# Kernel optimization log

Hardware: AMD Instinct MI355X
Metric: run time of the kernel (lower is better)

## Reference

```python
import jax, jax.numpy as jnp
import numpy as np

EMBED = 1024
HEADS = 16
HEAD_DIM = EMBED // HEADS


def setup_inputs() -> dict:
    key = jax.random.key(0)
    ks = jax.random.split(key, 12)
    B, S, D = 4, 2048, EMBED
    scale = 1.0 / np.sqrt(D)
    inp = {
        "query": jax.random.normal(ks[0], (B, S, D), dtype=jnp.float32),
        "key": jax.random.normal(ks[1], (B, S, D), dtype=jnp.float32),
        "value": jax.random.normal(ks[2], (B, S, D), dtype=jnp.float32),
        "Wq": jax.random.normal(ks[3], (D, D), dtype=jnp.float32) * scale,
        "bq": jnp.zeros((D,), dtype=jnp.float32),
        "Wk": jax.random.normal(ks[4], (D, D), dtype=jnp.float32) * scale,
        "bk": jnp.zeros((D,), dtype=jnp.float32),
        "Wv": jax.random.normal(ks[5], (D, D), dtype=jnp.float32) * scale,
        "bv": jnp.zeros((D,), dtype=jnp.float32),
        "Wo": jax.random.normal(ks[6], (D, D), dtype=jnp.float32) * scale,
        "bo": jnp.zeros((D,), dtype=jnp.float32),
    }
    return inp


def reference(query, key, value, Wq, bq, Wk, bk, Wv, bv, Wo, bo):
    B, S, D = query.shape
    H, Dh = HEADS, HEAD_DIM

    def proj(x, W, b):
        # nn.Linear: x @ W.T + b, then split heads -> [B, H, S, Dh]
        y = jnp.einsum('bsd,ed->bse', x, W) + b
        return y.reshape(B, -1, H, Dh).transpose(0, 2, 1, 3)

    q = proj(query, Wq, bq)
    k = proj(key, Wk, bk)
    v = proj(value, Wv, bv)

    attn = jnp.einsum('bhqd,bhkd->bhqk', q, k) / jnp.sqrt(jnp.float32(Dh))
    attn = jax.nn.softmax(attn, axis=-1)
    # dropout: eval mode -> identity
    out = jnp.einsum('bhqk,bhkd->bhqd', attn, v)
    out = out.transpose(0, 2, 1, 3).reshape(B, -1, D)
    out = jnp.einsum('bsd,ed->bse', out, Wo) + bo
    return out
```

## Files before the change

### kernel.cpp

```cpp
#include <hip/hip_runtime.h>
#include <hip/hip_bf16.h>

typedef unsigned short u16;
typedef unsigned int u32;
typedef float f32x4 __attribute__((ext_vector_type(4)));
typedef float f32x16 __attribute__((ext_vector_type(16)));
typedef __bf16 bf16x8 __attribute__((ext_vector_type(8)));
typedef u32 u32x2 __attribute__((ext_vector_type(2)));

#define DEV static __device__ __forceinline__

DEV u16 f2b(float f) { __bf16 h = (__bf16)f; u16 r; __builtin_memcpy(&r, &h, 2); return r; }
DEV u32 pk2(float a, float b) { return (u32)f2b(a) | ((u32)f2b(b) << 16); }
DEV bf16x8 as_bf(uint4 v) { bf16x8 r; __builtin_memcpy(&r, &v, 16); return r; }

#define GLDS(g, l) __builtin_amdgcn_global_load_lds( \
    (__attribute__((address_space(1))) void*)(g),     \
    (__attribute__((address_space(3))) void*)(l), 16, 0, 0)

DEV void wb2() { asm volatile("s_waitcnt vmcnt(2)\n\ts_barrier" ::: "memory"); }
DEV void wb4() { asm volatile("s_waitcnt vmcnt(4)\n\ts_barrier" ::: "memory"); }
DEV void wb0() { asm volatile("s_waitcnt vmcnt(0)\n\ts_barrier" ::: "memory"); }

__global__ __launch_bounds__(256) void conva3_k(const float* __restrict__ s0,
                                                const float* __restrict__ s1,
                                                const float* __restrict__ s2,
                                                u16* __restrict__ dst, int n8)
{
  const int seg = blockIdx.y;
  const float* s = seg == 0 ? s0 : (seg == 1 ? s1 : s2);
  u16* d = dst + (size_t)seg * 8388608;
  const int stride = gridDim.x * 256;
  for (int i = blockIdx.x * 256 + threadIdx.x; i < n8; i += stride) {
    const float4* p = (const float4*)(s + (size_t)i * 8);
    const float4 a = p[0], b = p[1];
    *(uint4*)(d + (size_t)i * 8) =
        make_uint4(pk2(a.x, a.y), pk2(a.z, a.w), pk2(b.x, b.y), pk2(b.z, b.w));
  }
}

__global__ __launch_bounds__(256) void convw_k(const float* __restrict__ w0,
                                               const float* __restrict__ w1,
                                               const float* __restrict__ w2,
                                               const float* __restrict__ w3,
                                               u16* __restrict__ dst)
{
  const int seg = blockIdx.x >> 9, sb = blockIdx.x & 511;
  const float* s = seg == 0 ? w0 : seg == 1 ? w1 : seg == 2 ? w2 : w3;
  const int i = sb * 256 + threadIdx.x;
  const float4* p = (const float4*)(s + (size_t)i * 8);
  const float4 a = p[0], b = p[1];
  *(uint4*)(dst + (size_t)seg * 1048576 + (size_t)i * 8) =
      make_uint4(pk2(a.x, a.y), pk2(a.z, a.w), pk2(b.x, b.y), pk2(b.z, b.w));
}

__global__ __launch_bounds__(256) void gemm_qkv(const u16* __restrict__ Ac,
                                                const u16* __restrict__ Wc,
                                                const float* __restrict__ b0,
                                                const float* __restrict__ b1,
                                                const float* __restrict__ b2,
                                                u16* __restrict__ C0,
                                                u16* __restrict__ C1,
                                                u16* __restrict__ C2,
                                                float qscale, int zq, int zv)
{
  __shared__ u16 lds[3][8192];
  const int tid = threadIdx.x;
  const int lane = tid & 63, w = tid >> 6;
  const int z = blockIdx.z;
  const int m0 = blockIdx.x * 128, e0 = blockIdx.y * 128;
  const int wrb = (w >> 1) * 4, wcb = (w & 1) * 4;

  const u16* A = Ac + (size_t)z * 8388608;
  const u16* Wp = Wc + (size_t)z * 1048576;
  const float* bias = z == 0 ? b0 : (z == 1 ? b1 : b2);
  u16* Cp = z == 0 ? C0 : (z == 1 ? C1 : C2);
  const float scale = (z == zq) ? qscale : 1.0f;
  const int cmode = (z == zv) ? 3 : 2;

  f32x4 acc[4][4];
#pragma unroll
  for (int i = 0; i < 4; i++)
#pragma unroll
    for (int j = 0; j < 4; j++)
#pragma unroll
      for (int r = 0; r < 4; r++) acc[i][j][r] = 0.f;

  const u16* gA = A  + (size_t)(m0 + w * 32 + (lane & 15)) * 1024 + (lane >> 4) * 8;
  const u16* gB = Wp + (size_t)(e0 + w * 32 + (lane & 15)) * 1024 + (lane >> 4) * 8;

#define GSTAGE(K0, BUF)                                        \
  GLDS(gA + (K0),         &lds[BUF][w * 1024]);                \
  GLDS(gA + (K0) + 16384, &lds[BUF][w * 1024 + 512]);          \
  GLDS(gB + (K0),         &lds[BUF][4096 + w * 1024]);         \
  GLDS(gB + (K0) + 16384, &lds[BUF][4096 + w * 1024 + 512]);

  GSTAGE(0, 0)
  GSTAGE(32, 1)

  const int fo = (lane >> 4) * 128 + (lane & 15) * 8;

#define GEMM_STEP(BUF)                                                         \
  {                                                                            \
    const u16* la = &lds[BUF][0];                                              \
    const u16* lb = &lds[BUF][4096];                                           \
    bf16x8 af[4], bfr[4];                                                      \
    _Pragma("unroll")                                                          \
    for (int i = 0; i < 4; i++) {                                              \
      af[i]  = as_bf(*(const uint4*)(la + (wrb + i) * 512 + fo));              \
      bfr[i] = as_bf(*(const uint4*)(lb + (wcb + i) * 512 + fo));              \
    }                                                                          \
    _Pragma("unroll")                                                          \
    for (int i = 0; i < 4; i++)                                                \
      _Pragma("unroll")                                                        \
      for (int j = 0; j < 4; j++)                                              \
        acc[i][j] = __builtin_amdgcn_mfma_f32_16x16x32_bf16(af[i], bfr[j],     \
                                                            acc[i][j], 0, 0, 0); \
  }

  for (int t = 0; t < 30; t += 3) {
    wb4(); GSTAGE((t + 2) * 32, 2) GEMM_STEP(0)
    wb4(); GSTAGE((t + 3) * 32, 0) GEMM_STEP(1)
    wb4(); GSTAGE((t + 4) * 32, 1) GEMM_STEP(2)
  }
  wb4(); GEMM_STEP(0)
  wb0(); GEMM_STEP(1)
#undef GEMM_STEP
#undef GSTAGE

  const int col = lane & 15, rb4 = (lane >> 4) * 4;
  const int wr = wrb * 16, wc = wcb * 16;
#pragma unroll
  for (int j = 0; j < 4; j++) {
    const int e = e0 + wc + j * 16 + col;
    const float bv2 = bias[e];
#pragma unroll
    for (int i = 0; i < 4; i++) {
#pragma unroll
      for (int r = 0; r < 4; r++) {
        const int m = m0 + wr + i * 16 + rb4 + r;
        const float v = (acc[i][j][r] + bv2) * scale;
        const int b = m >> 11, s = m & 2047, h = e >> 6, dh = e & 63;
        const size_t bh = (size_t)(b * 16 + h);
        if (cmode == 2) {
          const size_t idx = (((bh * 64 + (s >> 5)) * 4 + (dh >> 4)) * 64
                              + ((dh >> 3) & 1) * 32 + (s & 31)) * 8 + (dh & 7);
          Cp[idx] = f2b(v);
        } else {
          const size_t idx = ((bh * 64 + (s >> 5)) * 8 + ((s >> 4) & 1) * 4
                              + (dh >> 5) * 2 + ((s >> 3) & 1)) * 256
                             + (size_t)(dh & 31) * 8 + (s & 7);
          Cp[idx] = f2b(v);
        }
      }
    }
  }
}

__global__ __launch_bounds__(256) void gemm_o(const u16* __restrict__ A,
                                              const u16* __restrict__ W,
                                              const float* __restrict__ bias,
                                              float* __restrict__ Cp)
{
  __shared__ u16 lds[3][8192];
  const int tid = threadIdx.x;
  const int lane = tid & 63, w = tid >> 6;
  const int m0 = blockIdx.x * 128, e0 = blockIdx.y * 128;
  const int wrb = (w >> 1) * 4, wcb = (w & 1) * 4;

  f32x4 acc[4][4];
#pragma unroll
  for (int i = 0; i < 4; i++)
#pragma unroll
    for (int j = 0; j < 4; j++)
#pragma unroll
      for (int r = 0; r < 4; r++) acc[i][j][r] = 0.f;

  const u16* gA = A + (size_t)(m0 + w * 32 + (lane & 15)) * 1024 + (lane >> 4) * 8;
  const u16* gB = W + (size_t)(e0 + w * 32 + (lane & 15)) * 1024 + (lane >> 4) * 8;

#define GSTAGE(K0, BUF)                                        \
  GLDS(gA + (K0),         &lds[BUF][w * 1024]);                \
  GLDS(gA + (K0) + 16384, &lds[BUF][w * 1024 + 512]);          \
  GLDS(gB + (K0),         &lds[BUF][4096 + w * 1024]);         \
  GLDS(gB + (K0) + 16384, &lds[BUF][4096 + w * 1024 + 512]);

  GSTAGE(0, 0)
  GSTAGE(32, 1)

  const int fo = (lane >> 4) * 128 + (lane & 15) * 8;

#define GEMM_STEP(BUF)                                                         \
  {                                                                            \
    const u16* la = &lds[BUF][0];                                              \
    const u16* lb = &lds[BUF][4096];                                           \
    bf16x8 af[4], bfr[4];                                                      \
    _Pragma("unroll")                                                          \
    for (int i = 0; i < 4; i++) {                                              \
      af[i]  = as_bf(*(const uint4*)(la + (wrb + i) * 512 + fo));              \
      bfr[i] = as_bf(*(const uint4*)(lb + (wcb + i) * 512 + fo));              \
    }                                                                          \
    _Pragma("unroll")                                                          \
    for (int i = 0; i < 4; i++)                                                \
      _Pragma("unroll")                                                        \
      for (int j = 0; j < 4; j++)                                              \
        acc[i][j] = __builtin_amdgcn_mfma_f32_16x16x32_bf16(af[i], bfr[j],     \
                                                            acc[i][j], 0, 0, 0); \
  }

  for (int t = 0; t < 30; t += 3) {
    wb4(); GSTAGE((t + 2) * 32, 2) GEMM_STEP(0)
    wb4(); GSTAGE((t + 3) * 32, 0) GEMM_STEP(1)
    wb4(); GSTAGE((t + 4) * 32, 1) GEMM_STEP(2)
  }
  wb4(); GEMM_STEP(0)
  wb0(); GEMM_STEP(1)
#undef GEMM_STEP
#undef GSTAGE

  const int col = lane & 15, rb4 = (lane >> 4) * 4;
  const int wr = wrb * 16, wc = wcb * 16;
#pragma unroll
  for (int j = 0; j < 4; j++) {
    const int e = e0 + wc + j * 16 + col;
    const float bv = bias[e];
#pragma unroll
    for (int i = 0; i < 4; i++) {
#pragma unroll
      for (int r = 0; r < 4; r++) {
        const int m = m0 + wr + i * 16 + rb4 + r;
        Cp[(size_t)m * 1024 + e] = acc[i][j][r] + bv;
      }
    }
  }
}

__global__ __launch_bounds__(256, 4) void attn_k(const u16* __restrict__ Qb,
                                                 const u16* __restrict__ Kb,
                                                 const u16* __restrict__ Vb,
                                                 u16* __restrict__ O)
{
  __shared__ u16 pool[12288];
  const int tid = threadIdx.x, wv = tid >> 6, lane = tid & 63;
  const int lo = lane & 31, hi = lane >> 5;
  const int bid = blockIdx.x;
  const int xcd = bid & 7, ix = bid >> 3;
  const int bh = xcd * 8 + (ix & 7);
  const int qb = (ix >> 3) * 4 + wv;
  const int b = bh >> 4, h = bh & 15, q0 = qb * 32;

  const u16* qp = Qb + ((size_t)(bh * 64 + qb) * 4) * 512 + (size_t)lane * 8;
  bf16x8 qf[4];
#pragma unroll
  for (int c = 0; c < 4; c++) qf[c] = as_bf(*(const uint4*)(qp + c * 512));

  f32x16 a0, a1, zv;
#pragma unroll
  for (int r = 0; r < 16; r++) { a0[r] = 0.f; a1[r] = 0.f; zv[r] = 0.f; }
  float ls0 = 0.f, ls1 = 0.f;

  const u16* sgK = Kb + (size_t)bh * 131072 + wv * 512 + (size_t)lane * 8;
  const u16* sgV = Vb + (size_t)bh * 131072 + wv * 512 + (size_t)lane * 8;

#define ASTAGE(T, BUF)                                                  \
  GLDS(sgK + (size_t)(T) * 2048, pool + (BUF) * 4096 + wv * 512);       \
  GLDS(sgV + (size_t)(T) * 2048, pool + (BUF) * 4096 + 2048 + wv * 512);

  ASTAGE(0, 0)
  ASTAGE(1, 1)

#define ATTN_STEP(BUF)                                                        \
  {                                                                           \
    const u16* kl = pool + (BUF) * 4096;                                      \
    const u16* vl = kl + 2048;                                                \
    __builtin_amdgcn_s_setprio(1);                                            \
    f32x16 s = __builtin_amdgcn_mfma_f32_32x32x16_bf16(                       \
                 as_bf(*(const uint4*)(kl + lane * 8)), qf[0], zv, 0, 0, 0);  \
    _Pragma("unroll")                                                         \
    for (int c = 1; c < 4; c++)                                               \
      s = __builtin_amdgcn_mfma_f32_32x32x16_bf16(                            \
            as_bf(*(const uint4*)(kl + c * 512 + lane * 8)), qf[c], s, 0, 0, 0); \
    __builtin_amdgcn_s_setprio(0);                                            \
    _Pragma("unroll")                                                         \
    for (int r = 0; r < 16; r++) s[r] = __builtin_amdgcn_exp2f(s[r]);         \
    _Pragma("unroll")                                                         \
    for (int r = 0; r < 16; r += 2) { ls0 += s[r]; ls1 += s[r + 1]; }         \
    bf16x8 pf[2];                                                             \
    _Pragma("unroll")                                                         \
    for (int kc = 0; kc < 2; kc++) {                                          \
      const u32 A0 = pk2(s[8 * kc + 0], s[8 * kc + 1]);                       \
      const u32 A1 = pk2(s[8 * kc + 2], s[8 * kc + 3]);                       \
      const u32 B0 = pk2(s[8 * kc + 4], s[8 * kc + 5]);                       \
      const u32 B1 = pk2(s[8 * kc + 6], s[8 * kc + 7]);                       \
      u32x2 w02 = __builtin_amdgcn_permlane32_swap(A0, B0, false, false);     \
      u32x2 w13 = __builtin_amdgcn_permlane32_swap(A1, B1, false, false);     \
      pf[kc] = as_bf(make_uint4(w02[0], w13[0], w02[1], w13[1]));             \
    }                                                                         \
    __builtin_amdgcn_s_setprio(1);                                            \
    a0 = __builtin_amdgcn_mfma_f32_32x32x16_bf16(                             \
           as_bf(*(const uint4*)(vl + 0    + lane * 8)), pf[0], a0, 0, 0, 0); \
    a1 = __builtin_amdgcn_mfma_f32_32x32x16_bf16(                             \
           as_bf(*(const uint4*)(vl + 512  + lane * 8)), pf[0], a1, 0, 0, 0); \
    a0 = __builtin_amdgcn_mfma_f32_32x32x16_bf16(                             \
           as_bf(*(const uint4*)(vl + 1024 + lane * 8)), pf[1], a0, 0, 0, 0); \
    a1 = __builtin_amdgcn_mfma_f32_32x32x16_bf16(                             \
           as_bf(*(const uint4*)(vl + 1536 + lane * 8)), pf[1], a1, 0, 0, 0); \
    __builtin_amdgcn_s_setprio(0);                                            \
  }

  for (int t = 0; t < 60; t += 3) {
    wb2(); ASTAGE(t + 2, 2) ATTN_STEP(0)
    wb2(); ASTAGE(t + 3, 0) ATTN_STEP(1)
    wb2(); ASTAGE(t + 4, 1) ATTN_STEP(2)
  }
  wb2(); ASTAGE(62, 2) ATTN_STEP(0)
  wb2(); ASTAGE(63, 0) ATTN_STEP(1)
  wb2(); ATTN_STEP(2)
  wb0(); ATTN_STEP(0)
#undef ATTN_STEP
#undef ASTAGE

  __syncthreads();

  float l = ls0 + ls1;
  l += __shfl_xor(l, 32);
  const float inv = 1.f / l;
  u16* ob = pool + (wv * 32) * 72;

#pragma unroll
  for (int r = 0; r < 16; r++) {
    const int dh = (r & 3) + 8 * (r >> 2) + 4 * hi;
    ob[lo * 72 + dh]      = f2b(a0[r] * inv);
    ob[lo * 72 + dh + 32] = f2b(a1[r] * inv);
  }
  __builtin_amdgcn_s_barrier();
  const int qr = lane >> 1, hf = lane & 1;
  const u16* src = ob + qr * 72 + hf * 32;
  const uint4 r0 = *(const uint4*)(src + 0);
  const uint4 r1 = *(const uint4*)(src + 8);
  const uint4 r2 = *(const uint4*)(src + 16);
  const uint4 r3 = *(const uint4*)(src + 24);
  const size_t m = (size_t)b * 2048 + q0 + qr;
  uint4* dst = (uint4*)(O + m * 1024 + (size_t)h * 64 + hf * 32);
  dst[0] = r0; dst[1] = r1; dst[2] = r2; dst[3] = r3;
}

extern "C" void kernel_launch(void* const* d_in, const int* in_sizes, int n_in,
                              void* d_out, int out_size, void* d_ws, size_t ws_size,
                              hipStream_t stream)
{
  const float* query = (const float*)d_in[0];
  const float* key   = (const float*)d_in[1];
  const float* value = (const float*)d_in[2];
  const float* Wq = (const float*)d_in[3];
  const float* bq = (const float*)d_in[4];
  const float* Wk = (const float*)d_in[5];
  const float* bk = (const float*)d_in[6];
  const float* Wv = (const float*)d_in[7];
  const float* bv = (const float*)d_in[8];
  const float* Wo = (const float*)d_in[9];
  const float* bo = (const float*)d_in[10];

  const size_t MAT = (size_t)8192 * 1024;
  const size_t WMAT = (size_t)1024 * 1024;
  const float qscale = 0.125f * 1.4426950408889634f;
  dim3 bl(256, 1, 1);

  if (ws_size >= (6 * MAT + 4 * WMAT) * sizeof(u16)) {
    u16* Ac3 = (u16*)d_ws;
    u16* Wc  = Ac3 + 3 * MAT;
    u16* Qw  = Wc + 4 * WMAT;
    u16* Kw  = Qw + MAT;
    u16* Vw  = Kw + MAT;
    u16* Ow  = Ac3;

    hipLaunchKernelGGL(convw_k, dim3(2048), bl, 0, stream, Wq, Wk, Wv, Wo, Wc);
    hipLaunchKernelGGL(conva3_k, dim3(2048, 3), bl, 0, stream,
                       query, key, value, Ac3, (int)(MAT / 8));
    hipLaunchKernelGGL(gemm_qkv, dim3(64, 8, 3), bl, 0, stream,
                       Ac3, Wc, bq, bk, bv, Qw, Kw, Vw, qscale, 0, 2);
    hipLaunchKernelGGL(attn_k, dim3(1024), bl, 0, stream, Qw, Kw, Vw, Ow);
    hipLaunchKernelGGL(gemm_o, dim3(64, 8), bl, 0, stream,
                       Ow, Wc + 3 * WMAT, bo, (float*)d_out);
  } else {
    u16* Ac = (u16*)d_ws;
    u16* Wc = Ac + MAT;
    u16* Qw = Wc + 4 * WMAT;
    u16* Kw = Qw + MAT;
    u16* Vw = Kw + MAT;
    u16* Ow = Ac;
    if (ws_size < (4 * MAT + 4 * WMAT) * sizeof(u16)) return;

    hipLaunchKernelGGL(convw_k, dim3(2048), bl, 0, stream, Wq, Wk, Wv, Wo, Wc);

    hipLaunchKernelGGL(conva3_k, dim3(2048, 1), bl, 0, stream,
                       query, query, query, Ac, (int)(MAT / 8));
    hipLaunchKernelGGL(gemm_qkv, dim3(64, 8, 1), bl, 0, stream,
                       Ac, Wc + 0 * WMAT, bq, bq, bq, Qw, Qw, Qw, qscale, 0, -1);

    hipLaunchKernelGGL(conva3_k, dim3(2048, 1), bl, 0, stream,
                       key, key, key, Ac, (int)(MAT / 8));
    hipLaunchKernelGGL(gemm_qkv, dim3(64, 8, 1), bl, 0, stream,
                       Ac, Wc + 1 * WMAT, bk, bk, bk, Kw, Kw, Kw, qscale, -1, -1);

    hipLaunchKernelGGL(conva3_k, dim3(2048, 1), bl, 0, stream,
                       value, value, value, Ac, (int)(MAT / 8));
    hipLaunchKernelGGL(gemm_qkv, dim3(64, 8, 1), bl, 0, stream,
                       Ac, Wc + 2 * WMAT, bv, bv, bv, Vw, Vw, Vw, qscale, -1, 0);

    hipLaunchKernelGGL(attn_k, dim3(1024), bl, 0, stream, Qw, Kw, Vw, Ow);
    hipLaunchKernelGGL(gemm_o, dim3(64, 8), bl, 0, stream,
                       Ow, Wc + 3 * WMAT, bo, (float*)d_out);
  }
}
```

Baseline: 257.7 us.

## Use XCD-aware 1D grid and simpler double-buffered K loop in QKV GEMM

Remaps the QKV projection GEMM to a 1D grid whose block index is decoded so that each XCD gets a contiguous group of M tiles sharing A rows, aiming at better L2 reuse. It also replaces the triple-buffered LDS pipeline, which used explicit vmcnt waits, with a double-buffered loop that issues a __syncthreads per K step. The low-workspace fallback path is removed. The simpler pipeline may expose more load latency because the barrier waits for every outstanding load each iteration.

```diff
diff --git a/kernel.cpp b/kernel.cpp
--- a/kernel.cpp
+++ b/kernel.cpp
@@ -62,29 +62,32 @@
                                                 u16* __restrict__ C0,
                                                 u16* __restrict__ C1,
                                                 u16* __restrict__ C2,
-                                                float qscale, int zq, int zv)
-{
-  __shared__ u16 lds[3][8192];
+                                                float qscale)
+{
+  __shared__ u16 lds[2][8192];
   const int tid = threadIdx.x;
   const int lane = tid & 63, w = tid >> 6;
-  const int z = blockIdx.z;
-  const int m0 = blockIdx.x * 128, e0 = blockIdx.y * 128;
+  const int f = blockIdx.x;
+  const int xcd = f & 7, i = f >> 3;
+  const int mg = i & 7, yz = i >> 3;
+  const int m0 = (xcd * 8 + mg) * 128;
+  const int z = yz >> 3, e0 = (yz & 7) * 128;
   const int wrb = (w >> 1) * 4, wcb = (w & 1) * 4;
 
   const u16* A = Ac + (size_t)z * 8388608;
   const u16* Wp = Wc + (size_t)z * 1048576;
   const float* bias = z == 0 ? b0 : (z == 1 ? b1 : b2);
   u16* Cp = z == 0 ? C0 : (z == 1 ? C1 : C2);
-  const float scale = (z == zq) ? qscale : 1.0f;
-  const int cmode = (z == zv) ? 3 : 2;
+  const float scale = (z == 0) ? qscale : 1.0f;
+  const int cmode = (z == 2) ? 3 : 2;
 
   f32x4 acc[4][4];
 #pragma unroll
-  for (int i = 0; i < 4; i++)
+  for (int ii = 0; ii < 4; ii++)
 #pragma unroll
     for (int j = 0; j < 4; j++)
 #pragma unroll
-      for (int r = 0; r < 4; r++) acc[i][j][r] = 0.f;
+      for (int r = 0; r < 4; r++) acc[ii][j][r] = 0.f;
 
   const u16* gA = A  + (size_t)(m0 + w * 32 + (lane & 15)) * 1024 + (lane >> 4) * 8;
   const u16* gB = Wp + (size_t)(e0 + w * 32 + (lane & 15)) * 1024 + (lane >> 4) * 8;
@@ -96,36 +99,32 @@
   GLDS(gB + (K0) + 16384, &lds[BUF][4096 + w * 1024 + 512]);
 
   GSTAGE(0, 0)
-  GSTAGE(32, 1)
+  __syncthreads();
 
   const int fo = (lane >> 4) * 128 + (lane & 15) * 8;
-
-#define GEMM_STEP(BUF)                                                         \
-  {                                                                            \
-    const u16* la = &lds[BUF][0];                                              \
-    const u16* lb = &lds[BUF][4096];                                           \
-    bf16x8 af[4], bfr[4];                                                      \
-    _Pragma("unroll")                                                          \
-    for (int i = 0; i < 4; i++) {                                              \
-      af[i]  = as_bf(*(const uint4*)(la + (wrb + i) * 512 + fo));              \
-      bfr[i] = as_bf(*(const uint4*)(lb + (wcb + i) * 512 + fo));              \
-    }                                                                          \
-    _Pragma("unroll")                                                          \
-    for (int i = 0; i < 4; i++)                                                \
-      _Pragma("unroll")                                                        \
-      for (int j = 0; j < 4; j++)                                              \
-        acc[i][j] = __builtin_amdgcn_mfma_f32_16x16x32_bf16(af[i], bfr[j],     \
-                                                            acc[i][j], 0, 0, 0); \
-  }
-
-  for (int t = 0; t < 30; t += 3) {
-    wb4(); GSTAGE((t + 2) * 32, 2) GEMM_STEP(0)
-    wb4(); GSTAGE((t + 3) * 32, 0) GEMM_STEP(1)
-    wb4(); GSTAGE((t + 4) * 32, 1) GEMM_STEP(2)
-  }
-  wb4(); GEMM_STEP(0)
-  wb0(); GEMM_STEP(1)
-#undef GEMM_STEP
+  int buf = 0;
+  for (int kb = 0; kb < 32; ++kb) {
+    const int nbuf = buf ^ 1;
+    if (kb < 31) { GSTAGE((kb + 1) * 32, nbuf) }
+    {
+      const u16* la = &lds[buf][0];
+      const u16* lb = &lds[buf][4096];
+      bf16x8 af[4], bfr[4];
+#pragma unroll
+      for (int ii = 0; ii < 4; ii++) {
+        af[ii]  = as_bf(*(const uint4*)(la + (wrb + ii) * 512 + fo));
+        bfr[ii] = as_bf(*(const uint4*)(lb + (wcb + ii) * 512 + fo));
+      }
+#pragma unroll
+      for (int ii = 0; ii < 4; ii++)
+#pragma unroll
+        for (int j = 0; j < 4; j++)
+          acc[ii][j] = __builtin_amdgcn_mfma_f32_16x16x32_bf16(af[ii], bfr[j],
+                                                               acc[ii][j], 0, 0, 0);
+    }
+    __syncthreads();
+    buf = nbuf;
+  }
 #undef GSTAGE
 
   const int col = lane & 15, rb4 = (lane >> 4) * 4;
@@ -135,11 +134,11 @@
     const int e = e0 + wc + j * 16 + col;
     const float bv2 = bias[e];
 #pragma unroll
-    for (int i = 0; i < 4; i++) {
+    for (int ii = 0; ii < 4; ii++) {
 #pragma unroll
       for (int r = 0; r < 4; r++) {
-        const int m = m0 + wr + i * 16 + rb4 + r;
-        const float v = (acc[i][j][r] + bv2) * scale;
+        const int m = m0 + wr + ii * 16 + rb4 + r;
+        const float v = (acc[ii][j][r] + bv2) * scale;
         const int b = m >> 11, s = m & 2047, h = e >> 6, dh = e & 63;
         const size_t bh = (size_t)(b * 16 + h);
         if (cmode == 2) {
@@ -363,53 +362,23 @@
 
   const size_t MAT = (size_t)8192 * 1024;
   const size_t WMAT = (size_t)1024 * 1024;
+  if (ws_size < (6 * MAT + 4 * WMAT) * sizeof(u16)) return;
+  u16* Ac3 = (u16*)d_ws;
+  u16* Wc  = Ac3 + 3 * MAT;
+  u16* Qw  = Wc + 4 * WMAT;
+  u16* Kw  = Qw + MAT;
+  u16* Vw  = Kw + MAT;
+  u16* Ow  = Ac3;
+
   const float qscale = 0.125f * 1.4426950408889634f;
   dim3 bl(256, 1, 1);
 
-  if (ws_size >= (6 * MAT + 4 * WMAT) * sizeof(u16)) {
-    u16* Ac3 = (u16*)d_ws;
-    u16* Wc  = Ac3 + 3 * MAT;
-    u16* Qw  = Wc + 4 * WMAT;
-    u16* Kw  = Qw + MAT;
-    u16* Vw  = Kw + MAT;
-    u16* Ow  = Ac3;
-
-    hipLaunchKernelGGL(convw_k, dim3(2048), bl, 0, stream, Wq, Wk, Wv, Wo, Wc);
-    hipLaunchKernelGGL(conva3_k, dim3(2048, 3), bl, 0, stream,
-                       query, key, value, Ac3, (int)(MAT / 8));
-    hipLaunchKernelGGL(gemm_qkv, dim3(64, 8, 3), bl, 0, stream,
-                       Ac3, Wc, bq, bk, bv, Qw, Kw, Vw, qscale, 0, 2);
-    hipLaunchKernelGGL(attn_k, dim3(1024), bl, 0, stream, Qw, Kw, Vw, Ow);
-    hipLaunchKernelGGL(gemm_o, dim3(64, 8), bl, 0, stream,
-                       Ow, Wc + 3 * WMAT, bo, (float*)d_out);
-  } else {
-    u16* Ac = (u16*)d_ws;
-    u16* Wc = Ac + MAT;
-    u16* Qw = Wc + 4 * WMAT;
-    u16* Kw = Qw + MAT;
-    u16* Vw = Kw + MAT;
-    u16* Ow = Ac;
-    if (ws_size < (4 * MAT + 4 * WMAT) * sizeof(u16)) return;
-
-    hipLaunchKernelGGL(convw_k, dim3(2048), bl, 0, stream, Wq, Wk, Wv, Wo, Wc);
-
-    hipLaunchKernelGGL(conva3_k, dim3(2048, 1), bl, 0, stream,
-                       query, query, query, Ac, (int)(MAT / 8));
-    hipLaunchKernelGGL(gemm_qkv, dim3(64, 8, 1), bl, 0, stream,
-                       Ac, Wc + 0 * WMAT, bq, bq, bq, Qw, Qw, Qw, qscale, 0, -1);
-
-    hipLaunchKernelGGL(conva3_k, dim3(2048, 1), bl, 0, stream,
-                       key, key, key, Ac, (int)(MAT / 8));
-    hipLaunchKernelGGL(gemm_qkv, dim3(64, 8, 1), bl, 0, stream,
-                       Ac, Wc + 1 * WMAT, bk, bk, bk, Kw, Kw, Kw, qscale, -1, -1);
-
-    hipLaunchKernelGGL(conva3_k, dim3(2048, 1), bl, 0, stream,
-                       value, value, value, Ac, (int)(MAT / 8));
-    hipLaunchKernelGGL(gemm_qkv, dim3(64, 8, 1), bl, 0, stream,
-                       Ac, Wc + 2 * WMAT, bv, bv, bv, Vw, Vw, Vw, qscale, -1, 0);
-
-    hipLaunchKernelGGL(attn_k, dim3(1024), bl, 0, stream, Qw, Kw, Vw, Ow);
-    hipLaunchKernelGGL(gemm_o, dim3(64, 8), bl, 0, stream,
-                       Ow, Wc + 3 * WMAT, bo, (float*)d_out);
-  }
-}
+  hipLaunchKernelGGL(convw_k, dim3(2048), bl, 0, stream, Wq, Wk, Wv, Wo, Wc);
+  hipLaunchKernelGGL(conva3_k, dim3(2048, 3), bl, 0, stream,
+                     query, key, value, Ac3, (int)(MAT / 8));
+  hipLaunchKernelGGL(gemm_qkv, dim3(1536), bl, 0, stream,
+                     Ac3, Wc, bq, bk, bv, Qw, Kw, Vw, qscale);
+  hipLaunchKernelGGL(attn_k, dim3(1024), bl, 0, stream, Qw, Kw, Vw, Ow);
+  hipLaunchKernelGGL(gemm_o, dim3(64, 8), bl, 0, stream,
+                     Ow, Wc + 3 * WMAT, bo, (float*)d_out);
+}
```

After: 255.6 us. About the same (-0.8%).
